# Kernel optimization log

Measured on AMD Instinct MI355X. Metric: run time of the kernel, lower is better.

## Reference

```python
import jax, jax.numpy as jnp
import numpy as np

B, G, N_IN, N_HID, N_OUT = 2, 4096, 8, 32, 32
ALPHA, BETA, BN_EPS = 0.005, 5e-5, 1e-5
EDGE_P = 0.05  # adjacency density


def _lin_init(k, fan_in, fan_out):
    k1, k2 = jax.random.split(k)
    lim = 1.0 / np.sqrt(fan_in)
    W = jax.random.uniform(k1, (fan_in, fan_out), minval=-lim, maxval=lim, dtype=jnp.float32)
    b = jax.random.uniform(k2, (fan_out,), minval=-lim, maxval=lim, dtype=jnp.float32)
    return W, b


def setup_inputs() -> dict:
    key = jax.random.key(0)
    ks = jax.random.split(key, 12)
    W_infer, b_infer = _lin_init(ks[0], N_IN, N_HID)
    W_e1, b_e1 = _lin_init(ks[1], 2 * N_HID, 1)
    W_e2, b_e2 = _lin_init(ks[2], 2 * N_HID, 1)
    W_n1, b_n1 = _lin_init(ks[3], 2 * N_HID, N_OUT)
    W_n2, b_n2 = _lin_init(ks[4], 2 * N_HID, N_OUT)
    W_m1, b_m1 = _lin_init(ks[5], 2 * N_HID, N_OUT)
    W_m2, b_m2 = _lin_init(ks[6], 2 * N_HID, N_OUT)
    x = jax.random.normal(ks[7], (B, G, N_IN), dtype=jnp.float32)
    edges1 = jax.random.bernoulli(ks[8], EDGE_P, (G, G)).astype(jnp.float32)
    edges2 = jax.random.bernoulli(ks[9], EDGE_P, (G, G)).astype(jnp.float32)
    bn_gamma = jnp.ones((G,), jnp.float32)
    bn_beta = jnp.zeros((G,), jnp.float32)
    return dict(x=x, edges1=edges1, edges2=edges2, W_infer=W_infer, b_infer=b_infer,
                W_e1=W_e1, b_e1=b_e1, W_e2=W_e2, b_e2=b_e2,
                W_n1=W_n1, b_n1=b_n1, W_n2=W_n2, b_n2=b_n2,
                W_m1=W_m1, b_m1=b_m1, W_m2=W_m2, b_m2=b_m2,
                bn_gamma=bn_gamma, bn_beta=bn_beta)


def _mp_block(x, adj, coef, W_e, b_e, W_n, b_n, W_m, b_m):
    # x: [B,G,H]. Torch builds edge feature at flat index k=i*G+j as cat([x_j, x_i])
    # (shape2 = col gather, shape1 = row gather). We keep the same math without
    # materializing the [B,G*G,2H] tensor.
    Hh = x.shape[-1]
    s_src = x @ W_e[:Hh]   # [B,G,1]  (x_j part of mlp_edge)
    s_dst = x @ W_e[Hh:]   # [B,G,1]  (x_i part of mlp_edge)
    logits = s_dst[:, :, None, 0] + s_src[:, None, :, 0] + b_e[0]   # [B,G,G] at (i,j)
    w = adj + coef * (adj == 0).astype(x.dtype)                     # ori_edge + coef*thres_edge
    e = jax.nn.sigmoid(logits) * w[None]                            # [B,G,G]
    # receive at node i: sum_j e_ij * [x_j, x_i]
    recv_src = jnp.einsum('bij,bjh->bih', e, x)                     # sum_j e_ij x_j
    recv_dst = x * jnp.sum(e, axis=2)[..., None]                    # x_i * sum_j e_ij
    recv = jnp.concatenate([recv_src, recv_dst], axis=-1)           # [B,G,2H]
    recv = jax.nn.elu(recv @ W_n + b_n)                             # nodes_mlp + elu
    upd = jnp.concatenate([recv, x], axis=-1) @ W_m + b_m           # mesg_merge (mode='cat')
    return jax.nn.elu(upd)


def _forward(x, edges1, edges2, W_infer, b_infer, W_e1, b_e1, W_e2, b_e2,
             W_n1, b_n1, W_n2, b_n2, W_m1, b_m1, W_m2, b_m2, bn_gamma, bn_beta):
    h = jax.nn.elu(x @ W_infer + b_infer)                           # infer + elu, [B,G,H]
    h = _mp_block(h, edges1, ALPHA, W_e1, b_e1, W_n1, b_n1, W_m1, b_m1)
    # BatchNorm1d(gene_num) on [B, G, n_out]: per-gene stats over (batch, feature)
    mu = jnp.mean(h, axis=(0, 2), keepdims=True)
    var = jnp.var(h, axis=(0, 2), keepdims=True)
    h = (h - mu) * jax.lax.rsqrt(var + BN_EPS)
    h = h * bn_gamma[None, :, None] + bn_beta[None, :, None]
    return _mp_block(h, edges2, BETA, W_e2, b_e2, W_n2, b_n2, W_m2, b_m2)


def reference(x, edges1, edges2, W_infer, b_infer, W_e1, b_e1, W_e2, b_e2,
              W_n1, b_n1, W_n2, b_n2, W_m1, b_m1, W_m2, b_m2, bn_gamma, bn_beta):
    return _forward(x, edges1, edges2, W_infer, b_infer, W_e1, b_e1, W_e2, b_e2,
                    W_n1, b_n1, W_n2, b_n2, W_m1, b_m1, W_m2, b_m2, bn_gamma, bn_beta)
```

## Files before the change

kernel.cpp:

```cpp
#include <hip/hip_runtime.h>

#define G 4096
#define BSZ 2
#define NIN 8
#define HID 32
#define JS 8

typedef __attribute__((ext_vector_type(8))) short short8;
typedef __attribute__((ext_vector_type(4))) float floatx4;
typedef __attribute__((ext_vector_type(2))) short short2v;
typedef __attribute__((ext_vector_type(4))) short short4v;

__device__ __forceinline__ float elu1(float v) {
    return v > 0.f ? v : (__expf(v) - 1.f);
}
__device__ __forceinline__ unsigned short f2bf(float f) {
    unsigned u = __float_as_uint(f);
    u += 0x7fffu + ((u >> 16) & 1u);
    return (unsigned short)(u >> 16);
}

__global__ void k_setup1(const float* __restrict__ x, const float* __restrict__ W,
                         const float* __restrict__ bias, const float* __restrict__ We,
                         float* __restrict__ h0, unsigned short* __restrict__ hTb,
                         float* __restrict__ ssrc, float* __restrict__ sdst) {
    int t = blockIdx.x * blockDim.x + threadIdx.x;
    if (t >= BSZ * G) return;
    int b = t >> 12, g = t & (G - 1);
    float xin[NIN];
    const float* xp = x + t * NIN;
#pragma unroll
    for (int k = 0; k < NIN; k++) xin[k] = xp[k];
    float ss = 0.f, sd = 0.f;
    float* hp = h0 + (size_t)t * HID;
#pragma unroll
    for (int o = 0; o < HID; o++) {
        float v = bias[o];
#pragma unroll
        for (int k = 0; k < NIN; k++) v += xin[k] * W[k * HID + o];
        v = elu1(v);
        hp[o] = v;
        hTb[(size_t)(b * HID + o) * G + g] = f2bf(v);
        ss += v * We[o];
        sd += v * We[HID + o];
    }
    ssrc[t] = ss;
    sdst[t] = sd;
}

__global__ __launch_bounds__(256) void k_main(
    const float* __restrict__ adj, const float* __restrict__ ssrc,
    const float* __restrict__ sdst, const unsigned short* __restrict__ hTb,
    const float* __restrict__ bep, float coef, float* __restrict__ part) {
    int tid = threadIdx.x;
    int w = tid >> 6, l = tid & 63;
    int b = w >> 1, ihalf = w & 1;
    int i0 = blockIdx.x * 32;
    int jbase = blockIdx.y * (G / JS);
    int i = i0 + ihalf * 16 + (l & 15);
    int kg = l >> 4;
    float sd = sdst[b * G + i] + bep[0];
    floatx4 c0 = {0.f, 0.f, 0.f, 0.f}, c1 = {0.f, 0.f, 0.f, 0.f};
    float es = 0.f;
    const float* adjrow = adj + (size_t)i * G;
    const float* srow = ssrc + b * G;
    const unsigned short* hb0 = hTb + (size_t)(b * HID + (l & 15)) * G;
    const unsigned short* hb1 = hb0 + (size_t)16 * G;

    for (int jc = 0; jc < (G / JS / 32); jc++) {
        int j0 = jbase + jc * 32;
        int jme = j0 + kg * 8;
        float4 a0 = *(const float4*)(adjrow + jme);
        float4 a1 = *(const float4*)(adjrow + jme + 4);
        float4 s0 = *(const float4*)(srow + jme);
        float4 s1 = *(const float4*)(srow + jme + 4);
        float av[8] = {a0.x, a0.y, a0.z, a0.w, a1.x, a1.y, a1.z, a1.w};
        float sv[8] = {s0.x, s0.y, s0.z, s0.w, s1.x, s1.y, s1.z, s1.w};
        short8 af;
#pragma unroll
        for (int t = 0; t < 8; t++) {
            float wgt = (av[t] == 0.f) ? coef : av[t];
            float sg = __builtin_amdgcn_rcpf(1.f + __expf(-(sd + sv[t])));
            float e = sg * wgt;
            es += e;
            af[t] = (short)f2bf(e);
        }
        short8 bf0 = *(const short8*)(const void*)(hb0 + jme);
        short8 bf1 = *(const short8*)(const void*)(hb1 + jme);
        c0 = __builtin_amdgcn_mfma_f32_16x16x32_bf16(af, bf0, c0, 0, 0, 0);
        c1 = __builtin_amdgcn_mfma_f32_16x16x32_bf16(af, bf1, c1, 0, 0, 0);
    }
    es += __shfl_xor(es, 16);
    es += __shfl_xor(es, 32);
    size_t rb = ((size_t)(blockIdx.y * BSZ + b)) * G;
#pragma unroll
    for (int r = 0; r < 4; r++) {
        int row = i0 + ihalf * 16 + kg * 4 + r;
        part[(rb + row) * 33 + (l & 15)] = c0[r];
        part[(rb + row) * 33 + 16 + (l & 15)] = c1[r];
    }
    if (l < 16) part[(rb + i) * 33 + 32] = es;
}

template <bool DO_BN>
__global__ __launch_bounds__(256) void k_post(
    const float* __restrict__ part, const float* __restrict__ hin,
    const float* __restrict__ Wn, const float* __restrict__ bn,
    const float* __restrict__ Wm, const float* __restrict__ bm,
    const float* __restrict__ gamma, const float* __restrict__ beta,
    const float* __restrict__ We2, float* __restrict__ outp,
    unsigned short* __restrict__ hTb, float* __restrict__ s2s,
    float* __restrict__ s2d) {
    __shared__ float Wns[64 * 32];
    __shared__ float Wms[64 * 32];
    __shared__ float rec[8][68];
    __shared__ float rec2[8][68];
    __shared__ unsigned short tb[BSZ][HID][8];
    int tid = threadIdx.x;
    int rl = tid >> 5, hh = tid & 31;
    int wv = tid >> 6;
#pragma unroll
    for (int r = 0; r < 8; r++) {
        Wns[r * 256 + tid] = Wn[r * 256 + tid];
        Wms[r * 256 + tid] = Wm[r * 256 + tid];
    }
    __syncthreads();
    int g0 = blockIdx.x * 8;
    for (int rp = 0; rp < 2; rp++) {
        int rr = rp * 8 + rl;
        int b = rr & 1;
        int g = g0 + (rr >> 1);
        int rowf = b * G + g;
        float rs = 0.f, es = 0.f;
#pragma unroll
        for (int js = 0; js < JS; js++) {
            size_t base = ((size_t)(js * BSZ + b) * G + g) * 33;
            rs += part[base + hh];
            es += part[base + 32];
        }
        float xv = hin[(size_t)rowf * HID + hh];
        if (rp) __syncthreads();
        rec[rl][hh] = rs;
        rec[rl][32 + hh] = xv * es;
        __syncthreads();
        float v = bn[hh];
#pragma unroll
        for (int k4 = 0; k4 < 16; k4++) {
            float4 r4 = *(const float4*)&rec[rl][k4 * 4];
            v += r4.x * Wns[(k4 * 4 + 0) * HID + hh];
            v += r4.y * Wns[(k4 * 4 + 1) * HID + hh];
            v += r4.z * Wns[(k4 * 4 + 2) * HID + hh];
            v += r4.w * Wns[(k4 * 4 + 3) * HID + hh];
        }
        v = elu1(v);
        rec2[rl][hh] = v;
        rec2[rl][32 + hh] = xv;
        __syncthreads();
        float u = bm[hh];
#pragma unroll
        for (int k4 = 0; k4 < 16; k4++) {
            float4 r4 = *(const float4*)&rec2[rl][k4 * 4];
            u += r4.x * Wms[(k4 * 4 + 0) * HID + hh];
            u += r4.y * Wms[(k4 * 4 + 1) * HID + hh];
            u += r4.z * Wms[(k4 * 4 + 2) * HID + hh];
            u += r4.w * Wms[(k4 * 4 + 3) * HID + hh];
        }
        float h1v = elu1(u);
        if (!DO_BN) {
            outp[(size_t)rowf * HID + hh] = h1v;
        } else {
            float s = h1v, sq = h1v * h1v;
#pragma unroll
            for (int m = 32; m; m >>= 1) {
                s += __shfl_xor(s, m);
                sq += __shfl_xor(sq, m);
            }
            float mu = s * (1.f / 64.f);
            float var = sq * (1.f / 64.f) - mu * mu;
            float rstd = rsqrtf(var + 1e-5f);
            float hn = (h1v - mu) * rstd * gamma[g] + beta[g];
            outp[(size_t)rowf * HID + hh] = hn;
            tb[b][hh][rp * 4 + wv] = f2bf(hn);
            float ps = hn * We2[hh], pd = hn * We2[HID + hh];
#pragma unroll
            for (int m = 16; m; m >>= 1) {
                ps += __shfl_xor(ps, m);
                pd += __shfl_xor(pd, m);
            }
            if (hh == 0) {
                s2s[rowf] = ps;
                s2d[rowf] = pd;
            }
        }
    }
    if (DO_BN) {
        __syncthreads();
        int b2 = tid >> 7, c = (tid >> 2) & 31, g2 = (tid & 3) * 2;
        short2v val = *(const short2v*)&tb[b2][c][g2];
        *(short2v*)(void*)&hTb[(size_t)(b2 * HID + c) * G + g0 + g2] = val;
    }
}

extern "C" void kernel_launch(void* const* d_in, const int* in_sizes, int n_in,
                              void* d_out, int out_size, void* d_ws, size_t ws_size,
                              hipStream_t stream) {
    const float* x      = (const float*)d_in[0];
    const float* edges1 = (const float*)d_in[1];
    const float* edges2 = (const float*)d_in[2];
    const float* W_inf  = (const float*)d_in[3];
    const float* b_inf  = (const float*)d_in[4];
    const float* W_e1   = (const float*)d_in[5];
    const float* b_e1   = (const float*)d_in[6];
    const float* W_e2   = (const float*)d_in[7];
    const float* b_e2   = (const float*)d_in[8];
    const float* W_n1   = (const float*)d_in[9];
    const float* b_n1   = (const float*)d_in[10];
    const float* W_n2   = (const float*)d_in[11];
    const float* b_n2   = (const float*)d_in[12];
    const float* W_m1   = (const float*)d_in[13];
    const float* b_m1   = (const float*)d_in[14];
    const float* W_m2   = (const float*)d_in[15];
    const float* b_m2   = (const float*)d_in[16];
    const float* bn_g   = (const float*)d_in[17];
    const float* bn_b   = (const float*)d_in[18];
    float* out = (float*)d_out;

    float* ws = (float*)d_ws;
    float* h0   = ws;
    float* h1n  = ws + 262144;
    float* s1s  = ws + 524288;
    float* s1d  = ws + 532480;
    float* s2s  = ws + 540672;
    float* s2d  = ws + 548864;
    float* part = ws + 557056;
    unsigned short* hTb = (unsigned short*)(ws + 2719744);

    const float ALPHA = 0.005f, BETA = 5e-5f;

    k_setup1<<<32, 256, 0, stream>>>(x, W_inf, b_inf, W_e1, h0, hTb, s1s, s1d);
    k_main<<<dim3(G / 32, JS), 256, 0, stream>>>(edges1, s1s, s1d, hTb, b_e1, ALPHA, part);
    k_post<true><<<G / 8, 256, 0, stream>>>(part, h0, W_n1, b_n1, W_m1, b_m1,
                                            bn_g, bn_b, W_e2, h1n, hTb, s2s, s2d);
    k_main<<<dim3(G / 32, JS), 256, 0, stream>>>(edges2, s2s, s2d, hTb, b_e2, BETA, part);
    k_post<false><<<G / 8, 256, 0, stream>>>(part, h1n, W_n2, b_n2, W_m2, b_m2,
                                             nullptr, nullptr, nullptr, out,
                                             nullptr, nullptr, nullptr);
}
```

Measured before the change: 240.9 us.

## Increase j-split to 16, prefetch adjacency/features, simplify edge weight, halve post tile

The main edge-aggregation kernel now splits the j dimension into 16 chunks instead of 8, when workspace allows, to launch more blocks. Adjacency and feature loads are software-prefetched one iteration ahead. The weight select becomes an FMA, adj*(1-coef)+coef, which is only valid because adjacency is 0/1. The post kernel processes 4 genes per block instead of 8, so it launches twice as many blocks. The finer split raises the partial-sum buffer size and the reduction work in the post kernel.

Measured after the change: 265.2 us. +10.1%, slower.

```diff
diff --git a/kernel.cpp b/kernel.cpp
--- a/kernel.cpp
+++ b/kernel.cpp
@@ -4,25 +4,25 @@
 #define BSZ 2
 #define NIN 8
 #define HID 32
-#define JS 8
 
 typedef __attribute__((ext_vector_type(8))) short short8;
 typedef __attribute__((ext_vector_type(4))) float floatx4;
 typedef __attribute__((ext_vector_type(2))) short short2v;
 typedef __attribute__((ext_vector_type(4))) short short4v;
+typedef unsigned short ushort_t;
 
 __device__ __forceinline__ float elu1(float v) {
     return v > 0.f ? v : (__expf(v) - 1.f);
 }
-__device__ __forceinline__ unsigned short f2bf(float f) {
+__device__ __forceinline__ ushort_t f2bf(float f) {
     unsigned u = __float_as_uint(f);
     u += 0x7fffu + ((u >> 16) & 1u);
-    return (unsigned short)(u >> 16);
+    return (ushort_t)(u >> 16);
 }
 
 __global__ void k_setup1(const float* __restrict__ x, const float* __restrict__ W,
                          const float* __restrict__ bias, const float* __restrict__ We,
-                         float* __restrict__ h0, unsigned short* __restrict__ hTb,
+                         float* __restrict__ h0, ushort_t* __restrict__ hTb,
                          float* __restrict__ ssrc, float* __restrict__ sdst) {
     int t = blockIdx.x * blockDim.x + threadIdx.x;
     if (t >= BSZ * G) return;
@@ -50,43 +50,54 @@
 
 __global__ __launch_bounds__(256) void k_main(
     const float* __restrict__ adj, const float* __restrict__ ssrc,
-    const float* __restrict__ sdst, const unsigned short* __restrict__ hTb,
-    const float* __restrict__ bep, float coef, float* __restrict__ part) {
+    const float* __restrict__ sdst, const ushort_t* __restrict__ hTb,
+    const float* __restrict__ bep, float coef, float* __restrict__ part,
+    int chunk) {
     int tid = threadIdx.x;
     int w = tid >> 6, l = tid & 63;
     int b = w >> 1, ihalf = w & 1;
     int i0 = blockIdx.x * 32;
-    int jbase = blockIdx.y * (G / JS);
     int i = i0 + ihalf * 16 + (l & 15);
     int kg = l >> 4;
+    int jbase = blockIdx.y * chunk;
     float sd = sdst[b * G + i] + bep[0];
+    float wm1 = 1.f - coef;
+    const float* adjrow = adj + (size_t)i * G + jbase + kg * 8;
+    const float* srow = ssrc + b * G + jbase + kg * 8;
+    const ushort_t* hb0 = hTb + (size_t)(b * HID + (l & 15)) * G + jbase + kg * 8;
+    const ushort_t* hb1 = hb0 + (size_t)16 * G;
     floatx4 c0 = {0.f, 0.f, 0.f, 0.f}, c1 = {0.f, 0.f, 0.f, 0.f};
     float es = 0.f;
-    const float* adjrow = adj + (size_t)i * G;
-    const float* srow = ssrc + b * G;
-    const unsigned short* hb0 = hTb + (size_t)(b * HID + (l & 15)) * G;
-    const unsigned short* hb1 = hb0 + (size_t)16 * G;
-
-    for (int jc = 0; jc < (G / JS / 32); jc++) {
-        int j0 = jbase + jc * 32;
-        int jme = j0 + kg * 8;
-        float4 a0 = *(const float4*)(adjrow + jme);
-        float4 a1 = *(const float4*)(adjrow + jme + 4);
-        float4 s0 = *(const float4*)(srow + jme);
-        float4 s1 = *(const float4*)(srow + jme + 4);
+    int iters = chunk >> 5;
+
+    float4 pa0 = *(const float4*)(adjrow);
+    float4 pa1 = *(const float4*)(adjrow + 4);
+    short8 pb0 = *(const short8*)(const void*)(hb0);
+    short8 pb1 = *(const short8*)(const void*)(hb1);
+
+    for (int jc = 0; jc < iters; jc++) {
+        float4 a0 = pa0, a1 = pa1;
+        short8 bf0 = pb0, bf1 = pb1;
+        if (jc + 1 < iters) {
+            int o = (jc + 1) * 32;
+            pa0 = *(const float4*)(adjrow + o);
+            pa1 = *(const float4*)(adjrow + o + 4);
+            pb0 = *(const short8*)(const void*)(hb0 + o);
+            pb1 = *(const short8*)(const void*)(hb1 + o);
+        }
+        float4 s0 = *(const float4*)(srow + jc * 32);
+        float4 s1 = *(const float4*)(srow + jc * 32 + 4);
         float av[8] = {a0.x, a0.y, a0.z, a0.w, a1.x, a1.y, a1.z, a1.w};
         float sv[8] = {s0.x, s0.y, s0.z, s0.w, s1.x, s1.y, s1.z, s1.w};
         short8 af;
 #pragma unroll
         for (int t = 0; t < 8; t++) {
-            float wgt = (av[t] == 0.f) ? coef : av[t];
+            float wgt = __builtin_fmaf(av[t], wm1, coef);
             float sg = __builtin_amdgcn_rcpf(1.f + __expf(-(sd + sv[t])));
             float e = sg * wgt;
             es += e;
             af[t] = (short)f2bf(e);
         }
-        short8 bf0 = *(const short8*)(const void*)(hb0 + jme);
-        short8 bf1 = *(const short8*)(const void*)(hb1 + jme);
         c0 = __builtin_amdgcn_mfma_f32_16x16x32_bf16(af, bf0, c0, 0, 0, 0);
         c1 = __builtin_amdgcn_mfma_f32_16x16x32_bf16(af, bf1, c1, 0, 0, 0);
     }
@@ -105,99 +116,92 @@
 template <bool DO_BN>
 __global__ __launch_bounds__(256) void k_post(
     const float* __restrict__ part, const float* __restrict__ hin,
-    const float* __restrict__ Wn, const float* __restrict__ bn,
-    const float* __restrict__ Wm, const float* __restrict__ bm,
+    const float* __restrict__ Wn, const float* __restrict__ bnb,
+    const float* __restrict__ Wm, const float* __restrict__ bmb,
     const float* __restrict__ gamma, const float* __restrict__ beta,
     const float* __restrict__ We2, float* __restrict__ outp,
-    unsigned short* __restrict__ hTb, float* __restrict__ s2s,
-    float* __restrict__ s2d) {
+    ushort_t* __restrict__ hTb, float* __restrict__ s2s,
+    float* __restrict__ s2d, int jsn) {
     __shared__ float Wns[64 * 32];
     __shared__ float Wms[64 * 32];
     __shared__ float rec[8][68];
     __shared__ float rec2[8][68];
-    __shared__ unsigned short tb[BSZ][HID][8];
+    __shared__ ushort_t tb[BSZ][HID][4];
     int tid = threadIdx.x;
     int rl = tid >> 5, hh = tid & 31;
-    int wv = tid >> 6;
 #pragma unroll
     for (int r = 0; r < 8; r++) {
         Wns[r * 256 + tid] = Wn[r * 256 + tid];
         Wms[r * 256 + tid] = Wm[r * 256 + tid];
     }
+    int g0 = blockIdx.x * 4;
+    int b = rl & 1;
+    int g = g0 + (rl >> 1);
+    int rowf = b * G + g;
+    float rs = 0.f, es = 0.f;
+    for (int js = 0; js < jsn; js++) {
+        size_t base = ((size_t)(js * BSZ + b) * G + g) * 33;
+        rs += part[base + hh];
+        es += part[base + 32];
+    }
+    float xv = hin[(size_t)rowf * HID + hh];
+    rec[rl][hh] = rs;
+    rec[rl][32 + hh] = xv * es;
     __syncthreads();
-    int g0 = blockIdx.x * 8;
-    for (int rp = 0; rp < 2; rp++) {
-        int rr = rp * 8 + rl;
-        int b = rr & 1;
-        int g = g0 + (rr >> 1);
-        int rowf = b * G + g;
-        float rs = 0.f, es = 0.f;
-#pragma unroll
-        for (int js = 0; js < JS; js++) {
-            size_t base = ((size_t)(js * BSZ + b) * G + g) * 33;
-            rs += part[base + hh];
-            es += part[base + 32];
-        }
-        float xv = hin[(size_t)rowf * HID + hh];
-        if (rp) __syncthreads();
-        rec[rl][hh] = rs;
-        rec[rl][32 + hh] = xv * es;
+    float v = bnb[hh];
+#pragma unroll
+    for (int k4 = 0; k4 < 16; k4++) {
+        float4 r4 = *(const float4*)&rec[rl][k4 * 4];
+        v += r4.x * Wns[(k4 * 4 + 0) * HID + hh];
+        v += r4.y * Wns[(k4 * 4 + 1) * HID + hh];
+        v += r4.z * Wns[(k4 * 4 + 2) * HID + hh];
+        v += r4.w * Wns[(k4 * 4 + 3) * HID + hh];
+    }
+    v = elu1(v);
+    rec2[rl][hh] = v;
+    rec2[rl][32 + hh] = xv;
+    __syncthreads();
+    float u = bmb[hh];
+#pragma unroll
+    for (int k4 = 0; k4 < 16; k4++) {
+        float4 r4 = *(const float4*)&rec2[rl][k4 * 4];
+        u += r4.x * Wms[(k4 * 4 + 0) * HID + hh];
+        u += r4.y * Wms[(k4 * 4 + 1) * HID + hh];
+        u += r4.z * Wms[(k4 * 4 + 2) * HID + hh];
+        u += r4.w * Wms[(k4 * 4 + 3) * HID + hh];
+    }
+    float h1v = elu1(u);
+    if (!DO_BN) {
+        outp[(size_t)rowf * HID + hh] = h1v;
+    } else {
+        float s = h1v, sq = h1v * h1v;
+#pragma unroll
+        for (int m = 32; m; m >>= 1) {
+            s += __shfl_xor(s, m);
+            sq += __shfl_xor(sq, m);
+        }
+        float mu = s * (1.f / 64.f);
+        float var = sq * (1.f / 64.f) - mu * mu;
+        float rstd = rsqrtf(var + 1e-5f);
+        float hn = (h1v - mu) * rstd * gamma[g] + beta[g];
+        outp[(size_t)rowf * HID + hh] = hn;
+        tb[b][hh][rl >> 1] = f2bf(hn);
+        float ps = hn * We2[hh], pd = hn * We2[HID + hh];
+#pragma unroll
+        for (int m = 16; m; m >>= 1) {
+            ps += __shfl_xor(ps, m);
+            pd += __shfl_xor(pd, m);
+        }
+        if (hh == 0) {
+            s2s[rowf] = ps;
+            s2d[rowf] = pd;
+        }
         __syncthreads();
-        float v = bn[hh];
-#pragma unroll
-        for (int k4 = 0; k4 < 16; k4++) {
-            float4 r4 = *(const float4*)&rec[rl][k4 * 4];
-            v += r4.x * Wns[(k4 * 4 + 0) * HID + hh];
-            v += r4.y * Wns[(k4 * 4 + 1) * HID + hh];
-            v += r4.z * Wns[(k4 * 4 + 2) * HID + hh];
-            v += r4.w * Wns[(k4 * 4 + 3) * HID + hh];
-        }
-        v = elu1(v);
-        rec2[rl][hh] = v;
-        rec2[rl][32 + hh] = xv;
-        __syncthreads();
-        float u = bm[hh];
-#pragma unroll
-        for (int k4 = 0; k4 < 16; k4++) {
-            float4 r4 = *(const float4*)&rec2[rl][k4 * 4];
-            u += r4.x * Wms[(k4 * 4 + 0) * HID + hh];
-            u += r4.y * Wms[(k4 * 4 + 1) * HID + hh];
-            u += r4.z * Wms[(k4 * 4 + 2) * HID + hh];
-            u += r4.w * Wms[(k4 * 4 + 3) * HID + hh];
-        }
-        float h1v = elu1(u);
-        if (!DO_BN) {
-            outp[(size_t)rowf * HID + hh] = h1v;
-        } else {
-            float s = h1v, sq = h1v * h1v;
-#pragma unroll
-            for (int m = 32; m; m >>= 1) {
-                s += __shfl_xor(s, m);
-                sq += __shfl_xor(sq, m);
-            }
-            float mu = s * (1.f / 64.f);
-            float var = sq * (1.f / 64.f) - mu * mu;
-            float rstd = rsqrtf(var + 1e-5f);
-            float hn = (h1v - mu) * rstd * gamma[g] + beta[g];
-            outp[(size_t)rowf * HID + hh] = hn;
-            tb[b][hh][rp * 4 + wv] = f2bf(hn);
-            float ps = hn * We2[hh], pd = hn * We2[HID + hh];
-#pragma unroll
-            for (int m = 16; m; m >>= 1) {
-                ps += __shfl_xor(ps, m);
-                pd += __shfl_xor(pd, m);
-            }
-            if (hh == 0) {
-                s2s[rowf] = ps;
-                s2d[rowf] = pd;
-            }
-        }
-    }
-    if (DO_BN) {
-        __syncthreads();
-        int b2 = tid >> 7, c = (tid >> 2) & 31, g2 = (tid & 3) * 2;
-        short2v val = *(const short2v*)&tb[b2][c][g2];
-        *(short2v*)(void*)&hTb[(size_t)(b2 * HID + c) * G + g0 + g2] = val;
+        if (tid < 64) {
+            int b2 = tid >> 5, c = tid & 31;
+            short4v val = *(const short4v*)&tb[b2][c][0];
+            *(short4v*)(void*)&hTb[(size_t)(b2 * HID + c) * G + g0] = val;
+        }
     }
 }
 
@@ -233,16 +237,23 @@
     float* s2s  = ws + 540672;
     float* s2d  = ws + 548864;
     float* part = ws + 557056;
-    unsigned short* hTb = (unsigned short*)(ws + 2719744);
+
+    int JSN = 16;
+    size_t need16 = ((size_t)557056 + (size_t)16 * BSZ * G * 33 + 131072) * 4;
+    if (ws_size < need16) JSN = 8;
+    int chunk = G / JSN;
+    ushort_t* hTb = (ushort_t*)(part + (size_t)JSN * BSZ * G * 33);
 
     const float ALPHA = 0.005f, BETA = 5e-5f;
 
     k_setup1<<<32, 256, 0, stream>>>(x, W_inf, b_inf, W_e1, h0, hTb, s1s, s1d);
-    k_main<<<dim3(G / 32, JS), 256, 0, stream>>>(edges1, s1s, s1d, hTb, b_e1, ALPHA, part);
-    k_post<true><<<G / 8, 256, 0, stream>>>(part, h0, W_n1, b_n1, W_m1, b_m1,
-                                            bn_g, bn_b, W_e2, h1n, hTb, s2s, s2d);
-    k_main<<<dim3(G / 32, JS), 256, 0, stream>>>(edges2, s2s, s2d, hTb, b_e2, BETA, part);
-    k_post<false><<<G / 8, 256, 0, stream>>>(part, h1n, W_n2, b_n2, W_m2, b_m2,
+    k_main<<<dim3(G / 32, JSN), 256, 0, stream>>>(edges1, s1s, s1d, hTb, b_e1, ALPHA,
+                                                  part, chunk);
+    k_post<true><<<G / 4, 256, 0, stream>>>(part, h0, W_n1, b_n1, W_m1, b_m1,
+                                            bn_g, bn_b, W_e2, h1n, hTb, s2s, s2d, JSN);
+    k_main<<<dim3(G / 32, JSN), 256, 0, stream>>>(edges2, s2s, s2d, hTb, b_e2, BETA,
+                                                  part, chunk);
+    k_post<false><<<G / 4, 256, 0, stream>>>(part, h1n, W_n2, b_n2, W_m2, b_m2,
                                              nullptr, nullptr, nullptr, out,
-                                             nullptr, nullptr, nullptr);
-}
+                                             nullptr, nullptr, nullptr, JSN);
+}
```
